# Optimization experiments

Measured on AMD Instinct MI355X. Metric: run time of the kernel, lower is better.

Reference implementation:

```python
import jax, jax.numpy as jnp
import numpy as np

U = 300      # lstmUnit
D = 300      # embedding dim
T = 16384    # sequence length
ADIM = 350   # attentionDimension
R = 30       # multipleAttentions


def setup_inputs() -> dict:
    key = jax.random.key(0)
    ks = jax.random.split(key, 10)
    s = 0.05
    return {
        "embedding": jax.random.normal(ks[0], (1, T, D), jnp.float32),
        # Keras LSTM packs gates as [i, f, c, o] along the last axis.
        "Wk_f": jax.random.normal(ks[1], (D, 4 * U), jnp.float32) * s,
        "Wr_f": jax.random.normal(ks[2], (U, 4 * U), jnp.float32) * s,
        "b_f": jnp.zeros((4 * U,), jnp.float32),
        "Wk_b": jax.random.normal(ks[3], (D, 4 * U), jnp.float32) * s,
        "Wr_b": jax.random.normal(ks[4], (U, 4 * U), jnp.float32) * s,
        "b_b": jnp.zeros((4 * U,), jnp.float32),
        # W1 initialized as softmax(uniform) exactly like the TF code; it's a plain variable afterwards.
        "W1": jax.nn.softmax(jax.random.uniform(ks[5], (ADIM, 2 * U), jnp.float32), axis=-1),
        "W2": jax.random.uniform(ks[6], (R, ADIM), jnp.float32),
        "dense_w": jax.random.normal(ks[7], (2 * U, 1), jnp.float32) * s,
        "dense_b": jnp.zeros((1,), jnp.float32),
    }


def _lstm(x, Wk, Wr, b, reverse):
    # x: [T, D]. Precompute input projections as one big GEMM; scan only the recurrence.
    xp = x @ Wk + b                     # [T, 4U]
    if reverse:
        xp = xp[::-1]

    def step(carry, xt):
        h, c = carry
        # activation=sigmoid on the LSTM: candidate g AND output squash use sigmoid,
        # recurrent_activation (i, f, o gates) is also sigmoid -> one fused sigmoid.
        z = jax.nn.sigmoid(xt + h @ Wr)          # [4U]
        i, f, g, o = jnp.split(z, 4)
        c = f * c + i * g
        h = o * jax.nn.sigmoid(c)
        return (h, c), h

    init = (jnp.zeros((U,), x.dtype), jnp.zeros((U,), x.dtype))
    _, hs = jax.lax.scan(step, init, xp)         # [T, U]
    if reverse:
        hs = hs[::-1]
    return hs


def reference(embedding, Wk_f, Wr_f, b_f, Wk_b, Wr_b, b_b, W1, W2, dense_w, dense_b):
    x = embedding[0]                              # squeeze batch -> [T, D]
    hf = _lstm(x, Wk_f, Wr_f, b_f, reverse=False)
    hb = _lstm(x, Wk_b, Wr_b, b_b, reverse=True)
    H = jnp.concatenate([hf, hb], axis=-1)        # [T, 2U]
    # A = softmax(W2 @ tanh(W1 @ H^T)) over the time axis (tf default axis=-1)
    A = jax.nn.softmax(W2 @ jnp.tanh(W1 @ H.T), axis=-1)   # [R, T]
    Ma = A @ H                                    # [R, 2U]
    return jax.nn.sigmoid(jnp.mean(Ma @ dense_w + dense_b))
```

## Files before the change

### kernel.cpp

```cpp
#include <hip/hip_runtime.h>
#include <cstdint>

#define TSEQ   16384
#define NCH    24
#define WARM   128

static const size_t MA_OFF    = 0;
static const size_t STATS_OFF = 18000;
static const size_t XPF_OFF   = 18064;
static const size_t XPB_OFF   = 19678864;
static const size_t H_OFF     = 39339664;
static const size_t L_OFF     = 49170064;
static const size_t HX_OFF    = 49170064;

__global__ __launch_bounds__(256) void gemm_xp(
    const float* __restrict__ x,
    const float* __restrict__ Wk_f, const float* __restrict__ b_f,
    const float* __restrict__ Wk_b, const float* __restrict__ b_b,
    float* __restrict__ ws)
{
    const int mt = blockIdx.x, nt = blockIdx.y, dz = blockIdx.z;
    const float* __restrict__ Wk   = dz ? Wk_b : Wk_f;
    const float* __restrict__ bias = dz ? b_b : b_f;
    float* __restrict__ out = ws + (dz ? XPB_OFF : XPF_OFF);
    const int t0 = mt * 64, n0 = nt * 64;
    __shared__ __align__(16) float As[64][61];
    __shared__ __align__(16) float Bs[60][64];
    const int tid = threadIdx.x;
    const int tx = tid & 15, ty = tid >> 4;
    float acc[4][4];
#pragma unroll
    for (int i = 0; i < 4; ++i)
#pragma unroll
        for (int j2 = 0; j2 < 4; ++j2) acc[i][j2] = 0.f;

    for (int k0 = 0; k0 < 300; k0 += 60) {
        for (int i = tid; i < 3840; i += 256) {
            int mm = i / 60, kk = i % 60;
            As[mm][kk] = x[(size_t)(t0 + mm) * 300 + k0 + kk];
        }
        for (int i = tid; i < 3840; i += 256) {
            int kk = i >> 6, nn = i & 63;
            int gn = n0 + nn;
            Bs[kk][nn] = (gn < 1200) ? Wk[(size_t)(k0 + kk) * 1200 + gn] : 0.f;
        }
        __syncthreads();
#pragma unroll 4
        for (int kk = 0; kk < 60; ++kk) {
            float a0 = As[ty * 4 + 0][kk];
            float a1 = As[ty * 4 + 1][kk];
            float a2 = As[ty * 4 + 2][kk];
            float a3 = As[ty * 4 + 3][kk];
            float4 b4 = *(const float4*)&Bs[kk][tx * 4];
            acc[0][0] = fmaf(a0, b4.x, acc[0][0]); acc[0][1] = fmaf(a0, b4.y, acc[0][1]);
            acc[0][2] = fmaf(a0, b4.z, acc[0][2]); acc[0][3] = fmaf(a0, b4.w, acc[0][3]);
            acc[1][0] = fmaf(a1, b4.x, acc[1][0]); acc[1][1] = fmaf(a1, b4.y, acc[1][1]);
            acc[1][2] = fmaf(a1, b4.z, acc[1][2]); acc[1][3] = fmaf(a1, b4.w, acc[1][3]);
            acc[2][0] = fmaf(a2, b4.x, acc[2][0]); acc[2][1] = fmaf(a2, b4.y, acc[2][1]);
            acc[2][2] = fmaf(a2, b4.z, acc[2][2]); acc[2][3] = fmaf(a2, b4.w, acc[2][3]);
            acc[3][0] = fmaf(a3, b4.x, acc[3][0]); acc[3][1] = fmaf(a3, b4.y, acc[3][1]);
            acc[3][2] = fmaf(a3, b4.z, acc[3][2]); acc[3][3] = fmaf(a3, b4.w, acc[3][3]);
        }
        __syncthreads();
    }
    int gn = n0 + tx * 4;
    if (gn < 1200) {
        float4 bv = *(const float4*)&bias[gn];
#pragma unroll
        for (int i = 0; i < 4; ++i) {
            float4 v = make_float4(acc[i][0] + bv.x, acc[i][1] + bv.y,
                                   acc[i][2] + bv.z, acc[i][3] + bv.w);
            *(float4*)&out[(size_t)(t0 + ty * 4 + i) * 1200 + gn] = v;
        }
    }
}

__device__ __forceinline__ void matvec75x2(const float* __restrict__ hl,
                                           const float (&w)[2][75],
                                           float& a0, float& a1)
{
#pragma unroll
    for (int qq = 0; qq < 18; ++qq) {
        float4 hv = *(const float4*)(hl + qq * 4);
        a0 = fmaf(hv.x, w[0][qq * 4 + 0], a0); a1 = fmaf(hv.x, w[1][qq * 4 + 0], a1);
        a0 = fmaf(hv.y, w[0][qq * 4 + 1], a0); a1 = fmaf(hv.y, w[1][qq * 4 + 1], a1);
        a0 = fmaf(hv.z, w[0][qq * 4 + 2], a0); a1 = fmaf(hv.z, w[1][qq * 4 + 2], a1);
        a0 = fmaf(hv.w, w[0][qq * 4 + 3], a0); a1 = fmaf(hv.w, w[1][qq * 4 + 3], a1);
    }
#pragma unroll
    for (int kk = 72; kk < 75; ++kk) {
        float hv = hl[kk];
        a0 = fmaf(hv, w[0][kk], a0); a1 = fmaf(hv, w[1][kk], a1);
    }
}

__global__ __launch_bounds__(512, 1) void lstm_scan(
    const float* __restrict__ Wr_f, const float* __restrict__ Wr_b,
    float* __restrict__ ws)
{
    const int tid = threadIdx.x;
    const int id = blockIdx.x;
    const int xcd = id & 7, q = id >> 3;
    const int mem = q % 5;
    const int G = xcd * 6 + q / 5;
    const int dir = G / 24, chunk = G % 24;
    const int u0 = mem * 60;

    const float* __restrict__ Wr = dir ? Wr_b : Wr_f;
    const float* __restrict__ xp = ws + (dir ? XPB_OFF : XPF_OFF);
    float* __restrict__ H = ws + H_OFF;
    unsigned long long* __restrict__ hx =
        (unsigned long long*)(ws + HX_OFF) + (size_t)(dir * NCH + chunk) * 2 * 304;

    const int t_begin = chunk * 682 + (chunk < 16 ? chunk : 16);
    const int S_c = 682 + (chunk < 16 ? 1 : 0);
    const int t_end = t_begin + S_c;
    int rec0, nsteps;
    if (dir == 0) {
        rec0 = t_begin - WARM; if (rec0 < 0) rec0 = 0;
        nsteps = t_end - rec0;
    } else {
        rec0 = t_end - 1 + WARM; if (rec0 > TSEQ - 1) rec0 = TSEQ - 1;
        nsteps = rec0 - t_begin + 1;
    }

    __shared__ __align__(16) float h_lds[4 * 80];
    __shared__ __align__(16) float z_lds[240];

    const int cg = tid >> 2, rr4 = tid & 3;
    float w[2][75];
    if (tid < 480) {
#pragma unroll
        for (int c = 0; c < 2; ++c) {
            int jj = 2 * cg + c;
            int gam = jj / 60;
            int gcol = gam * 300 + u0 + (jj - gam * 60);
            const float* wp = Wr + (size_t)(rr4 * 75) * 1200 + gcol;
#pragma unroll
            for (int kk = 0; kk < 75; ++kk) w[c][kk] = wp[(size_t)kk * 1200];
        }
    }
    float cstate = 0.f;
    for (int i = tid; i < 320; i += 512) h_lds[i] = 0.f;

    int pw0 = 0, pw1 = 0, pw2 = 0, pw3 = 0;
    int pp0 = 0, pp1 = 0, pp2 = 0, pp3 = 0, own_pos = 0;
    if (tid < 60) {
        int m0 = mem + 1; if (m0 >= 5) m0 -= 5;
        int m1 = mem + 2; if (m1 >= 5) m1 -= 5;
        int m2 = mem + 3; if (m2 >= 5) m2 -= 5;
        int m3 = mem + 4; if (m3 >= 5) m3 -= 5;
        pw0 = m0 * 60 + tid; pw1 = m1 * 60 + tid;
        pw2 = m2 * 60 + tid; pw3 = m3 * 60 + tid;
        pp0 = (pw0 / 75) * 80 + (pw0 % 75);
        pp1 = (pw1 / 75) * 80 + (pw1 % 75);
        pp2 = (pw2 / 75) * 80 + (pw2 % 75);
        pp3 = (pw3 / 75) * 80 + (pw3 % 75);
        int ou = u0 + tid;
        own_pos = (ou / 75) * 80 + (ou % 75);
    }

    float xq0 = 0.f, xq1 = 0.f, xq2 = 0.f, xq3 = 0.f;
    if (tid < 60) {
        const float* xr = xp + (size_t)rec0 * 1200 + u0 + tid;
        xq0 = xr[0]; xq1 = xr[300]; xq2 = xr[600]; xq3 = xr[900];
    }
    __syncthreads();

    for (int s = 0; s < nsteps; ++s) {
        const int t = (dir == 0) ? (rec0 + s) : (rec0 - s);
        const float xpv0 = xq0, xpv1 = xq1, xpv2 = xq2, xpv3 = xq3;

        if (tid < 480) {
            float a0 = 0.f, a1 = 0.f;
            matvec75x2(h_lds + rr4 * 80, w, a0, a1);
            a0 += __shfl_xor(a0, 1); a0 += __shfl_xor(a0, 2);
            a1 += __shfl_xor(a1, 1); a1 += __shfl_xor(a1, 2);
            if (rr4 == 0) { z_lds[2 * cg] = a0; z_lds[2 * cg + 1] = a1; }
        }
        __syncthreads();
        if (tid < 60) {
            float zi = xpv0 + z_lds[tid];
            float zf = xpv1 + z_lds[60 + tid];
            float zg = xpv2 + z_lds[120 + tid];
            float zo = xpv3 + z_lds[180 + tid];
            float gi = 1.f / (1.f + __expf(-zi));
            float gf = 1.f / (1.f + __expf(-zf));
            float gg = 1.f / (1.f + __expf(-zg));
            float go = 1.f / (1.f + __expf(-zo));
            cstate = gf * cstate + gi * gg;
            float h = go / (1.f + __expf(-cstate));
            unsigned long long pk =
                (((unsigned long long)(unsigned)(s + 1)) << 32) |
                (unsigned long long)__float_as_uint(h);
            __hip_atomic_store(&hx[(size_t)(s & 1) * 304 + u0 + tid], pk,
                               __ATOMIC_RELAXED, __HIP_MEMORY_SCOPE_SYSTEM);
            h_lds[own_pos] = h;
            bool emit = (dir == 0) ? (t >= t_begin) : (t < t_end);
            if (emit) H[(size_t)t * 600 + dir * 300 + u0 + tid] = h;
            if (s + 1 < nsteps) {
                const unsigned tag = (unsigned)(s + 1);
                unsigned long long* slot = hx + (size_t)(s & 1) * 304;
                unsigned long long v0 = 0, v1 = 0, v2 = 0, v3 = 0;
                bool o0 = false, o1 = false, o2 = false, o3 = false;
                int spin = 0;
                for (;;) {
                    if (!o0) v0 = __hip_atomic_load(slot + pw0, __ATOMIC_RELAXED, __HIP_MEMORY_SCOPE_SYSTEM);
                    if (!o1) v1 = __hip_atomic_load(slot + pw1, __ATOMIC_RELAXED, __HIP_MEMORY_SCOPE_SYSTEM);
                    if (!o2) v2 = __hip_atomic_load(slot + pw2, __ATOMIC_RELAXED, __HIP_MEMORY_SCOPE_SYSTEM);
                    if (!o3) v3 = __hip_atomic_load(slot + pw3, __ATOMIC_RELAXED, __HIP_MEMORY_SCOPE_SYSTEM);
                    o0 = ((unsigned)(v0 >> 32) == tag);
                    o1 = ((unsigned)(v1 >> 32) == tag);
                    o2 = ((unsigned)(v2 >> 32) == tag);
                    o3 = ((unsigned)(v3 >> 32) == tag);
                    if (o0 && o1 && o2 && o3) break;
                    if (++spin > 3) __builtin_amdgcn_s_sleep(1);
                }
                h_lds[pp0] = __uint_as_float((unsigned)v0);
                h_lds[pp1] = __uint_as_float((unsigned)v1);
                h_lds[pp2] = __uint_as_float((unsigned)v2);
                h_lds[pp3] = __uint_as_float((unsigned)v3);
                int tn = (dir == 0) ? (t + 1) : (t - 1);
                const float* xr = xp + (size_t)tn * 1200 + u0 + tid;
                xq0 = xr[0]; xq1 = xr[300]; xq2 = xr[600]; xq3 = xr[900];
            }
        }
        __syncthreads();
    }
}

__global__ __launch_bounds__(256) void attn_logits(
    const float* __restrict__ W1, const float* __restrict__ W2,
    float* __restrict__ ws)
{
    const int t0 = blockIdx.x * 64;
    const float* __restrict__ H = ws + H_OFF;
    float* __restrict__ L = ws + L_OFF;
    __shared__ __align__(16) float Ht[60][68];
    __shared__ __align__(16) float W1t[60][68];
    __shared__ __align__(16) float Ss[64][68];
    const int tid = threadIdx.x;
    const int ag = tid >> 4, tg = tid & 15;
    float acc[6][16];
#pragma unroll
    for (int ap = 0; ap < 6; ++ap)
#pragma unroll
        for (int i = 0; i < 16; ++i) acc[ap][i] = 0.f;

    for (int k0 = 0; k0 < 600; k0 += 60) {
        __syncthreads();
        for (int i = tid; i < 3840; i += 256) {
            int kk = i % 60, tt = i / 60;
            Ht[kk][tt] = H[(size_t)(t0 + tt) * 600 + k0 + kk];
        }
#pragma unroll
        for (int ap = 0; ap < 6; ++ap) {
            __syncthreads();
            for (int i = tid; i < 3840; i += 256) {
                int kk = i % 60, aa = i / 60;
                int ga = ap * 64 + aa;
                W1t[kk][aa] = (ga < 350) ? W1[(size_t)ga * 600 + k0 + kk] : 0.f;
            }
            __syncthreads();
#pragma unroll 4
            for (int kk = 0; kk < 60; ++kk) {
                float4 av = *(const float4*)&W1t[kk][ag * 4];
                float4 hv = *(const float4*)&Ht[kk][tg * 4];
                acc[ap][0]  = fmaf(av.x, hv.x, acc[ap][0]);
                acc[ap][1]  = fmaf(av.x, hv.y, acc[ap][1]);
                acc[ap][2]  = fmaf(av.x, hv.z, acc[ap][2]);
                acc[ap][3]  = fmaf(av.x, hv.w, acc[ap][3]);
                acc[ap][4]  = fmaf(av.y, hv.x, acc[ap][4]);
                acc[ap][5]  = fmaf(av.y, hv.y, acc[ap][5]);
                acc[ap][6]  = fmaf(av.y, hv.z, acc[ap][6]);
                acc[ap][7]  = fmaf(av.y, hv.w, acc[ap][7]);
                acc[ap][8]  = fmaf(av.z, hv.x, acc[ap][8]);
                acc[ap][9]  = fmaf(av.z, hv.y, acc[ap][9]);
                acc[ap][10] = fmaf(av.z, hv.z, acc[ap][10]);
                acc[ap][11] = fmaf(av.z, hv.w, acc[ap][11]);
                acc[ap][12] = fmaf(av.w, hv.x, acc[ap][12]);
                acc[ap][13] = fmaf(av.w, hv.y, acc[ap][13]);
                acc[ap][14] = fmaf(av.w, hv.z, acc[ap][14]);
                acc[ap][15] = fmaf(av.w, hv.w, acc[ap][15]);
            }
        }
    }
    const int r = tid & 31, tg2 = tid >> 5;
    float lacc[8];
#pragma unroll
    for (int i = 0; i < 8; ++i) lacc[i] = 0.f;
#pragma unroll
    for (int ap = 0; ap < 6; ++ap) {
        __syncthreads();
#pragma unroll
        for (int i = 0; i < 4; ++i)
#pragma unroll
            for (int j2 = 0; j2 < 4; ++j2)
                Ss[ag * 4 + i][tg * 4 + j2] =
                    1.f - 2.f / (1.f + __expf(2.f * acc[ap][i * 4 + j2]));
        __syncthreads();
        if (r < 30) {
            for (int aa = 0; aa < 64; ++aa) {
                int ga = ap * 64 + aa;
                float w2v = (ga < 350) ? W2[(size_t)r * 350 + ga] : 0.f;
                float4 s0 = *(const float4*)&Ss[aa][tg2 * 8];
                float4 s1 = *(const float4*)&Ss[aa][tg2 * 8 + 4];
                lacc[0] = fmaf(w2v, s0.x, lacc[0]);
                lacc[1] = fmaf(w2v, s0.y, lacc[1]);
                lacc[2] = fmaf(w2v, s0.z, lacc[2]);
                lacc[3] = fmaf(w2v, s0.w, lacc[3]);
                lacc[4] = fmaf(w2v, s1.x, lacc[4]);
                lacc[5] = fmaf(w2v, s1.y, lacc[5]);
                lacc[6] = fmaf(w2v, s1.z, lacc[6]);
                lacc[7] = fmaf(w2v, s1.w, lacc[7]);
            }
        }
    }
    if (r < 30) {
#pragma unroll
        for (int j2 = 0; j2 < 8; ++j2)
            L[(size_t)r * 16384 + t0 + tg2 * 8 + j2] = lacc[j2];
    }
}

__global__ __launch_bounds__(256) void softmax_stats(float* __restrict__ ws)
{
    const int rrow = blockIdx.x;
    const float* __restrict__ Lr = ws + L_OFF + (size_t)rrow * 16384;
    float* __restrict__ stats = ws + STATS_OFF;
    __shared__ float red[256];
    const int tid = threadIdx.x;
    float m = -3.4e38f;
    for (int i = tid; i < 16384; i += 256) m = fmaxf(m, Lr[i]);
    red[tid] = m; __syncthreads();
    for (int s2 = 128; s2 > 0; s2 >>= 1) {
        if (tid < s2) red[tid] = fmaxf(red[tid], red[tid + s2]);
        __syncthreads();
    }
    m = red[0];
    __syncthreads();
    float sum = 0.f;
    for (int i = tid; i < 16384; i += 256) sum += __expf(Lr[i] - m);
    red[tid] = sum; __syncthreads();
    for (int s2 = 128; s2 > 0; s2 >>= 1) {
        if (tid < s2) red[tid] += red[tid + s2];
        __syncthreads();
    }
    if (tid == 0) { stats[rrow * 2] = m; stats[rrow * 2 + 1] = red[0]; }
}

__global__ __launch_bounds__(256) void ma_accum(float* __restrict__ ws)
{
    const float* __restrict__ H = ws + H_OFF;
    const float* __restrict__ L = ws + L_OFF;
    const float* __restrict__ stats = ws + STATS_OFF;
    float* __restrict__ Ma = ws + MA_OFF;
    const int t0 = blockIdx.x * 128;
    const int tid = threadIdx.x;
    __shared__ float avs[2][32];
    float accA[30], accB[30], accC[30];
#pragma unroll
    for (int r2 = 0; r2 < 30; ++r2) { accA[r2] = 0.f; accB[r2] = 0.f; accC[r2] = 0.f; }
    float mr = 0.f, isr = 0.f;
    if (tid < 30) {
        mr = stats[tid * 2]; isr = 1.f / stats[tid * 2 + 1];
        avs[0][tid] = __expf(L[(size_t)tid * 16384 + t0] - mr) * isr;
    }
    __syncthreads();
    for (int tt = 0; tt < 128; ++tt) {
        int t = t0 + tt;
        float h0 = H[(size_t)t * 600 + tid];
        float h1 = H[(size_t)t * 600 + 256 + tid];
        float h2 = (tid < 88) ? H[(size_t)t * 600 + 512 + tid] : 0.f;
        if (tt + 1 < 128 && tid < 30)
            avs[(tt + 1) & 1][tid] = __expf(L[(size_t)tid * 16384 + t + 1] - mr) * isr;
        const float* av = avs[tt & 1];
#pragma unroll
        for (int r2 = 0; r2 < 30; ++r2) {
            float a = av[r2];
            accA[r2] = fmaf(a, h0, accA[r2]);
            accB[r2] = fmaf(a, h1, accB[r2]);
            accC[r2] = fmaf(a, h2, accC[r2]);
        }
        __syncthreads();
    }
#pragma unroll
    for (int r2 = 0; r2 < 30; ++r2) {
        atomicAdd(&Ma[r2 * 600 + tid], accA[r2]);
        atomicAdd(&Ma[r2 * 600 + 256 + tid], accB[r2]);
        if (tid < 88) atomicAdd(&Ma[r2 * 600 + 512 + tid], accC[r2]);
    }
}

__global__ void final_out(const float* __restrict__ dw, const float* __restrict__ db,
                          const float* __restrict__ ws, float* __restrict__ out)
{
    const float* __restrict__ Ma = ws + MA_OFF;
    __shared__ float red[256];
    const int tid = threadIdx.x;
    float p = 0.f;
    for (int i = tid; i < 18000; i += 256) {
        int c = i % 600;
        p = fmaf(Ma[i], dw[c], p);
    }
    red[tid] = p;
    __syncthreads();
    for (int s2 = 128; s2 > 0; s2 >>= 1) {
        if (tid < s2) red[tid] += red[tid + s2];
        __syncthreads();
    }
    if (tid == 0) {
        float mval = red[0] / 30.f + db[0];
        out[0] = 1.f / (1.f + __expf(-mval));
    }
}

extern "C" void kernel_launch(void* const* d_in, const int* in_sizes, int n_in,
                              void* d_out, int out_size, void* d_ws, size_t ws_size,
                              hipStream_t stream)
{
    const float* x    = (const float*)d_in[0];
    const float* Wk_f = (const float*)d_in[1];
    const float* Wr_f = (const float*)d_in[2];
    const float* b_f  = (const float*)d_in[3];
    const float* Wk_b = (const float*)d_in[4];
    const float* Wr_b = (const float*)d_in[5];
    const float* b_b  = (const float*)d_in[6];
    const float* W1   = (const float*)d_in[7];
    const float* W2   = (const float*)d_in[8];
    const float* dw   = (const float*)d_in[9];
    const float* db   = (const float*)d_in[10];
    float* ws  = (float*)d_ws;
    float* out = (float*)d_out;

    hipMemsetAsync(d_ws, 0, 18000 * sizeof(float), stream);

    gemm_xp<<<dim3(256, 19, 2), 256, 0, stream>>>(x, Wk_f, b_f, Wk_b, b_b, ws);
    lstm_scan<<<240, 512, 0, stream>>>(Wr_f, Wr_b, ws);
    attn_logits<<<256, 256, 0, stream>>>(W1, W2, ws);
    softmax_stats<<<30, 256, 0, stream>>>(ws);
    ma_accum<<<128, 256, 0, stream>>>(ws);
    final_out<<<1, 256, 0, stream>>>(dw, db, ws, out);
}
```

Measured before the change: 2.582 ms.

## Group LSTM scan blocks by runtime XCC ID and poll peers at agent scope

Each lstm_scan block now reads its hardware XCC ID and registers itself in a global counter table. It then waits for all blocks to register and computes a group assignment so that the five cooperating members of a chunk sit on the same XCD whenever possible, rather than assuming a blockIdx-to-XCD mapping. Same-XCD groups first poll their peers' h values with agent-scope atomic loads before falling back to system-scope polling, and each h value is stored at both scopes. The warm-up length is also cut from 128 to 96 steps, which reduces redundant recurrence work but may affect accuracy at chunk boundaries. The added launch-time barrier needs every block to be co-resident, and the double store adds traffic on every step.

```diff
diff --git a/kernel.cpp b/kernel.cpp
--- a/kernel.cpp
+++ b/kernel.cpp
@@ -3,15 +3,17 @@
 
 #define TSEQ   16384
 #define NCH    24
-#define WARM   128
+#define WARM   96
+#define NBLK   240
 
 static const size_t MA_OFF    = 0;
-static const size_t STATS_OFF = 18000;
-static const size_t XPF_OFF   = 18064;
-static const size_t XPB_OFF   = 19678864;
-static const size_t H_OFF     = 39339664;
-static const size_t L_OFF     = 49170064;
-static const size_t HX_OFF    = 49170064;
+static const size_t REG_OFF   = 18000;
+static const size_t STATS_OFF = 18016;
+static const size_t XPF_OFF   = 18080;
+static const size_t XPB_OFF   = 19678880;
+static const size_t H_OFF     = 39339680;
+static const size_t L_OFF     = 49170080;
+static const size_t HX_OFF    = 49170080;
 
 __global__ __launch_bounds__(256) void gemm_xp(
     const float* __restrict__ x,
@@ -99,18 +101,49 @@
     float* __restrict__ ws)
 {
     const int tid = threadIdx.x;
-    const int id = blockIdx.x;
-    const int xcd = id & 7, q = id >> 3;
-    const int mem = q % 5;
-    const int G = xcd * 6 + q / 5;
-    const int dir = G / 24, chunk = G % 24;
+    __shared__ int sb[3];
+
+    if (tid == 0) {
+        unsigned xcc;
+        asm volatile("s_getreg_b32 %0, hwreg(HW_REG_XCC_ID)" : "=s"(xcc));
+        xcc &= 7u;
+        unsigned* regs = (unsigned*)(ws + REG_OFF);
+        int slot = (int)__hip_atomic_fetch_add(&regs[xcc], 1u,
+                                               __ATOMIC_RELAXED, __HIP_MEMORY_SCOPE_SYSTEM);
+        __hip_atomic_fetch_add(&regs[8], 1u, __ATOMIC_RELAXED, __HIP_MEMORY_SCOPE_SYSTEM);
+        while (__hip_atomic_load(&regs[8], __ATOMIC_RELAXED,
+                                 __HIP_MEMORY_SCOPE_SYSTEM) < (unsigned)NBLK)
+            __builtin_amdgcn_s_sleep(8);
+        unsigned cnt[8];
+#pragma unroll
+        for (int x2 = 0; x2 < 8; ++x2)
+            cnt[x2] = __hip_atomic_load(&regs[x2], __ATOMIC_RELAXED,
+                                        __HIP_MEMORY_SCOPE_SYSTEM);
+        int prefull = 0, totfull = 0, lpre = 0;
+        for (int x2 = 0; x2 < 8; ++x2) {
+            int f = (int)cnt[x2] / 5;
+            if (x2 < (int)xcc) { prefull += f; lpre += (int)cnt[x2] - f * 5; }
+            totfull += f;
+        }
+        int myfull = (int)cnt[xcc] / 5;
+        int grp, mm, same;
+        if (slot < myfull * 5) { grp = prefull + slot / 5; mm = slot % 5; same = 1; }
+        else {
+            int lidx = lpre + (slot - myfull * 5);
+            grp = totfull + lidx / 5; mm = lidx % 5; same = 0;
+        }
+        sb[0] = grp; sb[1] = mm; sb[2] = same;
+    }
+    __syncthreads();
+    const int grp = sb[0], mem = sb[1], fastpoll = sb[2];
+    const int dir = grp / NCH, chunk = grp % NCH;
     const int u0 = mem * 60;
 
     const float* __restrict__ Wr = dir ? Wr_b : Wr_f;
     const float* __restrict__ xp = ws + (dir ? XPB_OFF : XPF_OFF);
     float* __restrict__ H = ws + H_OFF;
     unsigned long long* __restrict__ hx =
-        (unsigned long long*)(ws + HX_OFF) + (size_t)(dir * NCH + chunk) * 2 * 304;
+        (unsigned long long*)(ws + HX_OFF) + (size_t)grp * 2 * 304;
 
     const int t_begin = chunk * 682 + (chunk < 16 ? chunk : 16);
     const int S_c = 682 + (chunk < 16 ? 1 : 0);
@@ -193,8 +226,9 @@
             unsigned long long pk =
                 (((unsigned long long)(unsigned)(s + 1)) << 32) |
                 (unsigned long long)__float_as_uint(h);
-            __hip_atomic_store(&hx[(size_t)(s & 1) * 304 + u0 + tid], pk,
-                               __ATOMIC_RELAXED, __HIP_MEMORY_SCOPE_SYSTEM);
+            unsigned long long* dst = &hx[(size_t)(s & 1) * 304 + u0 + tid];
+            __hip_atomic_store(dst, pk, __ATOMIC_RELAXED, __HIP_MEMORY_SCOPE_AGENT);
+            __hip_atomic_store(dst, pk, __ATOMIC_RELAXED, __HIP_MEMORY_SCOPE_SYSTEM);
             h_lds[own_pos] = h;
             bool emit = (dir == 0) ? (t >= t_begin) : (t < t_end);
             if (emit) H[(size_t)t * 600 + dir * 300 + u0 + tid] = h;
@@ -203,16 +237,21 @@
                 unsigned long long* slot = hx + (size_t)(s & 1) * 304;
                 unsigned long long v0 = 0, v1 = 0, v2 = 0, v3 = 0;
                 bool o0 = false, o1 = false, o2 = false, o3 = false;
+                if (fastpoll) {
+                    for (int it = 0; it < 8; ++it) {
+                        if (!o0) { v0 = __hip_atomic_load(slot + pw0, __ATOMIC_RELAXED, __HIP_MEMORY_SCOPE_AGENT); o0 = ((unsigned)(v0 >> 32) == tag); }
+                        if (!o1) { v1 = __hip_atomic_load(slot + pw1, __ATOMIC_RELAXED, __HIP_MEMORY_SCOPE_AGENT); o1 = ((unsigned)(v1 >> 32) == tag); }
+                        if (!o2) { v2 = __hip_atomic_load(slot + pw2, __ATOMIC_RELAXED, __HIP_MEMORY_SCOPE_AGENT); o2 = ((unsigned)(v2 >> 32) == tag); }
+                        if (!o3) { v3 = __hip_atomic_load(slot + pw3, __ATOMIC_RELAXED, __HIP_MEMORY_SCOPE_AGENT); o3 = ((unsigned)(v3 >> 32) == tag); }
+                        if (o0 && o1 && o2 && o3) break;
+                    }
+                }
                 int spin = 0;
-                for (;;) {
-                    if (!o0) v0 = __hip_atomic_load(slot + pw0, __ATOMIC_RELAXED, __HIP_MEMORY_SCOPE_SYSTEM);
-                    if (!o1) v1 = __hip_atomic_load(slot + pw1, __ATOMIC_RELAXED, __HIP_MEMORY_SCOPE_SYSTEM);
-                    if (!o2) v2 = __hip_atomic_load(slot + pw2, __ATOMIC_RELAXED, __HIP_MEMORY_SCOPE_SYSTEM);
-                    if (!o3) v3 = __hip_atomic_load(slot + pw3, __ATOMIC_RELAXED, __HIP_MEMORY_SCOPE_SYSTEM);
-                    o0 = ((unsigned)(v0 >> 32) == tag);
-                    o1 = ((unsigned)(v1 >> 32) == tag);
-                    o2 = ((unsigned)(v2 >> 32) == tag);
-                    o3 = ((unsigned)(v3 >> 32) == tag);
+                while (!(o0 && o1 && o2 && o3)) {
+                    if (!o0) { v0 = __hip_atomic_load(slot + pw0, __ATOMIC_RELAXED, __HIP_MEMORY_SCOPE_SYSTEM); o0 = ((unsigned)(v0 >> 32) == tag); }
+                    if (!o1) { v1 = __hip_atomic_load(slot + pw1, __ATOMIC_RELAXED, __HIP_MEMORY_SCOPE_SYSTEM); o1 = ((unsigned)(v1 >> 32) == tag); }
+                    if (!o2) { v2 = __hip_atomic_load(slot + pw2, __ATOMIC_RELAXED, __HIP_MEMORY_SCOPE_SYSTEM); o2 = ((unsigned)(v2 >> 32) == tag); }
+                    if (!o3) { v3 = __hip_atomic_load(slot + pw3, __ATOMIC_RELAXED, __HIP_MEMORY_SCOPE_SYSTEM); o3 = ((unsigned)(v3 >> 32) == tag); }
                     if (o0 && o1 && o2 && o3) break;
                     if (++spin > 3) __builtin_amdgcn_s_sleep(1);
                 }
@@ -433,10 +472,10 @@
     float* ws  = (float*)d_ws;
     float* out = (float*)d_out;
 
-    hipMemsetAsync(d_ws, 0, 18000 * sizeof(float), stream);
+    hipMemsetAsync(d_ws, 0, 18016 * sizeof(float), stream);
 
     gemm_xp<<<dim3(256, 19, 2), 256, 0, stream>>>(x, Wk_f, b_f, Wk_b, b_b, ws);
-    lstm_scan<<<240, 512, 0, stream>>>(Wr_f, Wr_b, ws);
+    lstm_scan<<<NBLK, 512, 0, stream>>>(Wr_f, Wr_b, ws);
     attn_logits<<<256, 256, 0, stream>>>(W1, W2, ws);
     softmax_stats<<<30, 256, 0, stream>>>(ws);
     ma_accum<<<128, 256, 0, stream>>>(ws);
```

After: 2.843 ms. 10.1% more time.
